# Kernel tuning notes

Measured on AMD Instinct MI355X. Metric: run time of the kernel, lower is better.

Reference implementation:

```python
import jax, jax.numpy as jnp
import numpy as np

B, T = 16384, 128  # batch, n_frames


def setup_inputs() -> dict:
    key = jax.random.key(0)
    k0, k1, k2, k3, k4, k5 = jax.random.split(key, 6)
    dir = jax.random.normal(k0, (B, 3), dtype=jnp.float32)
    R = jax.random.normal(k1, (B, T, 3, 3), dtype=jnp.float32)
    s = 1.0 / np.sqrt(3.0)  # torch LSTM default init scale (uniform +-1/sqrt(hidden))
    W_ih = jax.random.uniform(k2, (12, 3), jnp.float32, -s, s)
    W_hh = jax.random.uniform(k3, (12, 3), jnp.float32, -s, s)
    b_ih = jax.random.uniform(k4, (12,), jnp.float32, -s, s)
    b_hh = jax.random.uniform(k5, (12,), jnp.float32, -s, s)
    return {"dir": dir, "R": R, "W_ih": W_ih, "W_hh": W_hh, "b_ih": b_ih, "b_hh": b_hh}


def _rot_step(v, Rm):
    # v: [B,3], Rm: [B,3,3] -> Rm @ v
    nv = jnp.einsum('bij,bj->bi', Rm, v)
    return nv, nv


def _build_dirs(dir, R):
    n_frames = R.shape[1]
    half = n_frames // 2
    # Backward chain: dirs[i] = R[half-1-i]^T @ ... @ R[half-1]^T @ dir
    Rt_back = jnp.swapaxes(jnp.flip(R[:, :half], axis=1), 2, 3)  # [B, half, 3, 3]
    _, back = jax.lax.scan(_rot_step, dir, jnp.swapaxes(Rt_back, 0, 1))  # [half, B, 3]
    # Forward chain: dirs[i] = R[i-1] @ ... @ R[half] @ dir for i in half+1..n-1
    Rf = jnp.swapaxes(R[:, half:n_frames - 1], 0, 1)  # [n-1-half, B, 3, 3]
    _, fwd = jax.lax.scan(_rot_step, dir, Rf)  # [n-1-half, B, 3]
    dirs_tm = jnp.concatenate([back, dir[None], fwd], axis=0)  # time-major [T, B, 3]
    return dirs_tm, half


def _lstm(dirs_tm, W_ih, W_hh, b_ih, b_hh):
    Bsz = dirs_tm.shape[1]
    h0 = jnp.zeros((Bsz, 3), dirs_tm.dtype)
    c0 = jnp.zeros((Bsz, 3), dirs_tm.dtype)
    bias = b_ih + b_hh

    def step(carry, x):
        h, c = carry
        gates = x @ W_ih.T + h @ W_hh.T + bias  # [B,12]
        i = jax.nn.sigmoid(gates[:, 0:3])
        f = jax.nn.sigmoid(gates[:, 3:6])
        g = jnp.tanh(gates[:, 6:9])
        o = jax.nn.sigmoid(gates[:, 9:12])
        c = f * c + i * g
        h = o * jnp.tanh(c)
        return (h, c), h

    _, h_seq = jax.lax.scan(step, (h0, c0), dirs_tm)  # [T, B, 3]
    return h_seq


def reference(dir, R, W_ih, W_hh, b_ih, b_hh):
    dirs_tm, half = _build_dirs(dir, R)
    h_seq = _lstm(dirs_tm, W_ih, W_hh, b_ih, b_hh)
    dirs_out = jnp.swapaxes(dirs_tm, 0, 1)  # [B, T, 3]
    return dirs_out.at[:, half, :].set(h_seq[half])
```

## Files before the change

kernel.cpp:

```cpp
#include <hip/hip_runtime.h>

typedef float f4 __attribute__((ext_vector_type(4)));
typedef float f4u __attribute__((ext_vector_type(4), aligned(4)));

struct M3 { float m[3][3]; };

#define ELEM(q, n) ((q)[(n) >> 2][(n) & 3])

__device__ __forceinline__ M3 matmul(const M3& A, const M3& B) {
  M3 C;
#pragma unroll
  for (int i = 0; i < 3; ++i)
#pragma unroll
    for (int j = 0; j < 3; ++j)
      C.m[i][j] = A.m[i][0]*B.m[0][j] + A.m[i][1]*B.m[1][j] + A.m[i][2]*B.m[2][j];
  return C;
}

__device__ __forceinline__ M3 mk18(const f4 (&q)[18], int k) {
  M3 A;
#pragma unroll
  for (int i = 0; i < 3; ++i)
#pragma unroll
    for (int j = 0; j < 3; ++j)
      A.m[i][j] = ELEM(q, 9*k + 3*i + j);
  return A;
}

template <int CTRL>
__device__ __forceinline__ float dppf(float v) {
  return __int_as_float(
      __builtin_amdgcn_mov_dpp(__float_as_int(v), CTRL, 0xf, 0xf, true));
}

template <int D>
__device__ __forceinline__ M3 dpp_shr_mat(const M3& A) {
  M3 C;
#pragma unroll
  for (int i = 0; i < 3; ++i)
#pragma unroll
    for (int j = 0; j < 3; ++j)
      C.m[i][j] = dppf<0x110 + D>(A.m[i][j]);
  return C;
}

__device__ __forceinline__ float sigm(float z) {
  return __builtin_amdgcn_rcpf(1.0f + __expf(-z));
}
__device__ __forceinline__ float tanh_(float z) {
  float e = __expf(2.0f * z);
  return 1.0f - 2.0f * __builtin_amdgcn_rcpf(e + 1.0f);
}

template <int CTRL>
__device__ __forceinline__ float quad_bcast(float v) {
  return __int_as_float(
      __builtin_amdgcn_mov_dpp(__float_as_int(v), CTRL, 0xf, 0xf, true));
}

__global__ __launch_bounds__(128, 2) void fused_kernel(
    const float* __restrict__ dir, const float* __restrict__ R,
    const float* __restrict__ Wih, const float* __restrict__ Whh,
    const float* __restrict__ bih, const float* __restrict__ bhh,
    float* __restrict__ out, int B) {
  __shared__ __align__(16) f4 xrows[64 * 16];

  const int tid = threadIdx.x;
  const int lane = tid & 63;
  const int e = tid >> 3;
  const int s = tid & 7;
  const int b0 = blockIdx.x * 16;
  const int b = b0 + e;
  const bool valid = (b < B);
  const int bc = valid ? b : (B - 1);
  const f4* Rb4 = (const f4*)(R + (size_t)bc * 1152);

  f4 q[18], qf[18];
  {
    const f4* pb = Rb4 + 18 * (7 - s);
    const f4* pf = Rb4 + 144 + 18 * s;
#pragma unroll
    for (int i = 0; i < 18; ++i) q[i] = pb[i];
#pragma unroll
    for (int i = 0; i < 18; ++i) qf[i] = pf[i];
  }
#pragma unroll
  for (int i = 0; i < 18; ++i) asm volatile("" :: "v"(q[i]));
#pragma unroll
  for (int i = 0; i < 18; ++i) asm volatile("" :: "v"(qf[i]));

  const float d0 = dir[3*bc+0], d1 = dir[3*bc+1], d2 = dir[3*bc+2];

  {
    M3 P = mk18(q, 0);
#pragma unroll
    for (int k = 1; k < 8; ++k) P = matmul(mk18(q, k), P);

    M3 I = P;
    {
      M3 Sh = dpp_shr_mat<1>(I); M3 T = matmul(Sh, I);
#pragma unroll
      for (int i = 0; i < 3; ++i)
#pragma unroll
        for (int j = 0; j < 3; ++j) I.m[i][j] = (s >= 1) ? T.m[i][j] : I.m[i][j];
    }
    {
      M3 Sh = dpp_shr_mat<2>(I); M3 T = matmul(Sh, I);
#pragma unroll
      for (int i = 0; i < 3; ++i)
#pragma unroll
        for (int j = 0; j < 3; ++j) I.m[i][j] = (s >= 2) ? T.m[i][j] : I.m[i][j];
    }
    {
      M3 Sh = dpp_shr_mat<4>(I); M3 T = matmul(Sh, I);
#pragma unroll
      for (int i = 0; i < 3; ++i)
#pragma unroll
        for (int j = 0; j < 3; ++j) I.m[i][j] = (s >= 4) ? T.m[i][j] : I.m[i][j];
    }

    float w0 = I.m[0][0]*d0 + I.m[1][0]*d1 + I.m[2][0]*d2;
    float w1 = I.m[0][1]*d0 + I.m[1][1]*d1 + I.m[2][1]*d2;
    float w2 = I.m[0][2]*d0 + I.m[1][2]*d1 + I.m[2][2]*d2;
    float p0 = dppf<0x111>(w0), p1 = dppf<0x111>(w1), p2 = dppf<0x111>(w2);
    float v0 = (s == 0) ? d0 : p0;
    float v1 = (s == 0) ? d1 : p1;
    float v2 = (s == 0) ? d2 : p2;

    float row[24];
#pragma unroll
    for (int j = 0; j < 8; ++j) {
      M3 A = mk18(q, 7 - j);
      float n0 = v0*A.m[0][0] + v1*A.m[1][0] + v2*A.m[2][0];
      float n1 = v0*A.m[0][1] + v1*A.m[1][1] + v2*A.m[2][1];
      float n2 = v0*A.m[0][2] + v1*A.m[1][2] + v2*A.m[2][2];
      v0 = n0; v1 = n1; v2 = n2;
      row[3*j+0] = n0; row[3*j+1] = n1; row[3*j+2] = n2;
    }

    if (valid) {
      float* ob = out + (size_t)b * 384 + 24 * s;
#pragma unroll
      for (int kk = 0; kk < 6; ++kk) {
        f4 vv = { row[4*kk+0], row[4*kk+1], row[4*kk+2], row[4*kk+3] };
        ((f4*)ob)[kk] = vv;
      }
    }
#pragma unroll
    for (int j = 0; j < 8; ++j) {
      f4 vv = { row[3*j+0], row[3*j+1], row[3*j+2], 0.f };
      xrows[(8*s + j) * 16 + e] = vv;
    }
  }

  {
    M3 P = mk18(qf, 0);
#pragma unroll
    for (int k = 1; k < 8; ++k) P = matmul(mk18(qf, k), P);

    M3 I = P;
    {
      M3 Sh = dpp_shr_mat<1>(I); M3 T = matmul(I, Sh);
#pragma unroll
      for (int i = 0; i < 3; ++i)
#pragma unroll
        for (int j = 0; j < 3; ++j) I.m[i][j] = (s >= 1) ? T.m[i][j] : I.m[i][j];
    }
    {
      M3 Sh = dpp_shr_mat<2>(I); M3 T = matmul(I, Sh);
#pragma unroll
      for (int i = 0; i < 3; ++i)
#pragma unroll
        for (int j = 0; j < 3; ++j) I.m[i][j] = (s >= 2) ? T.m[i][j] : I.m[i][j];
    }
    {
      M3 Sh = dpp_shr_mat<4>(I); M3 T = matmul(I, Sh);
#pragma unroll
      for (int i = 0; i < 3; ++i)
#pragma unroll
        for (int j = 0; j < 3; ++j) I.m[i][j] = (s >= 4) ? T.m[i][j] : I.m[i][j];
    }

    float w0 = I.m[0][0]*d0 + I.m[0][1]*d1 + I.m[0][2]*d2;
    float w1 = I.m[1][0]*d0 + I.m[1][1]*d1 + I.m[1][2]*d2;
    float w2 = I.m[2][0]*d0 + I.m[2][1]*d1 + I.m[2][2]*d2;
    float p0 = dppf<0x111>(w0), p1 = dppf<0x111>(w1), p2 = dppf<0x111>(w2);
    float v0 = (s == 0) ? d0 : p0;
    float v1 = (s == 0) ? d1 : p1;
    float v2 = (s == 0) ? d2 : p2;

    float row[24];
#pragma unroll
    for (int j = 0; j < 8; ++j) {
      M3 A = mk18(qf, j);
      float n0 = A.m[0][0]*v0 + A.m[0][1]*v1 + A.m[0][2]*v2;
      float n1 = A.m[1][0]*v0 + A.m[1][1]*v1 + A.m[1][2]*v2;
      float n2 = A.m[2][0]*v0 + A.m[2][1]*v1 + A.m[2][2]*v2;
      v0 = n0; v1 = n1; v2 = n2;
      row[3*j+0] = n0; row[3*j+1] = n1; row[3*j+2] = n2;
    }

    if (valid) {
      float* ob = out + (size_t)b * 384 + (size_t)(65 + 8*s) * 3;
#pragma unroll
      for (int kk = 0; kk < 5; ++kk) {
        f4u vv = { row[4*kk+0], row[4*kk+1], row[4*kk+2], row[4*kk+3] };
        *(f4u*)(ob + 4*kk) = vv;
      }
      ob[20] = row[20];
      if (s < 7) { ob[21] = row[21]; ob[22] = row[22]; ob[23] = row[23]; }
    }
  }

  __syncthreads();
  if (tid >= 64) return;

  const int e2 = lane >> 2;
  const int u = lane & 3, uu = (u == 3) ? 0 : u;
  const int b2 = b0 + e2;
  const bool valid2 = (b2 < B);
  const int b2c = valid2 ? b2 : 0;

  const float wii0 = Wih[uu*3+0],     wii1 = Wih[uu*3+1],     wii2 = Wih[uu*3+2];
  const float wif0 = Wih[(3+uu)*3+0], wif1 = Wih[(3+uu)*3+1], wif2 = Wih[(3+uu)*3+2];
  const float wig0 = Wih[(6+uu)*3+0], wig1 = Wih[(6+uu)*3+1], wig2 = Wih[(6+uu)*3+2];
  const float wio0 = Wih[(9+uu)*3+0], wio1 = Wih[(9+uu)*3+1], wio2 = Wih[(9+uu)*3+2];
  const float whi0 = Whh[uu*3+0],     whi1 = Whh[uu*3+1],     whi2 = Whh[uu*3+2];
  const float whf0 = Whh[(3+uu)*3+0], whf1 = Whh[(3+uu)*3+1], whf2 = Whh[(3+uu)*3+2];
  const float whg0 = Whh[(6+uu)*3+0], whg1 = Whh[(6+uu)*3+1], whg2 = Whh[(6+uu)*3+2];
  const float who0 = Whh[(9+uu)*3+0], who1 = Whh[(9+uu)*3+1], who2 = Whh[(9+uu)*3+2];
  const float bsi = bih[uu]   + bhh[uu];
  const float bsf = bih[3+uu] + bhh[3+uu];
  const float bsg = bih[6+uu] + bhh[6+uu];
  const float bso = bih[9+uu] + bhh[9+uu];
  const float dd0 = dir[3*b2c+0], dd1 = dir[3*b2c+1], dd2 = dir[3*b2c+2];

  float h0 = 0.f, h1 = 0.f, h2 = 0.f, cc = 0.f, hl = 0.f;

#define LSTEP(x0_, x1_, x2_)                                                  \
  {                                                                           \
    float zi = bsi + wii0*(x0_) + wii1*(x1_) + wii2*(x2_)                     \
                   + whi0*h0 + whi1*h1 + whi2*h2;                             \
    float zf = bsf + wif0*(x0_) + wif1*(x1_) + wif2*(x2_)                     \
                   + whf0*h0 + whf1*h1 + whf2*h2;                             \
    float zg = bsg + wig0*(x0_) + wig1*(x1_) + wig2*(x2_)                     \
                   + whg0*h0 + whg1*h1 + whg2*h2;                             \
    float zo = bso + wio0*(x0_) + wio1*(x1_) + wio2*(x2_)                     \
                   + who0*h0 + who1*h1 + who2*h2;                             \
    float ai = sigm(zi), af = sigm(zf), ag = tanh_(zg), ao = sigm(zo);        \
    cc = af*cc + ai*ag;                                                       \
    float hn = ao * tanh_(cc);                                                \
    hl = hn;                                                                  \
    h0 = quad_bcast<0x00>(hn);                                                \
    h1 = quad_bcast<0x55>(hn);                                                \
    h2 = quad_bcast<0xAA>(hn);                                                \
  }

#pragma unroll 1
  for (int c = 0; c < 8; ++c) {
    f4 xa[8];
#pragma unroll
    for (int j = 0; j < 8; ++j) xa[j] = xrows[(c * 8 + j) * 16 + e2];
#pragma unroll
    for (int j = 0; j < 8; ++j) LSTEP(xa[j][0], xa[j][1], xa[j][2]);
  }
  LSTEP(dd0, dd1, dd2);
#undef LSTEP

  if (valid2 && u < 3) out[(size_t)b2 * 384 + 192 + u] = hl;
}

extern "C" void kernel_launch(void* const* d_in, const int* in_sizes, int n_in,
                              void* d_out, int out_size, void* d_ws, size_t ws_size,
                              hipStream_t stream) {
  const float* dir = (const float*)d_in[0];
  const float* R   = (const float*)d_in[1];
  const float* Wih = (const float*)d_in[2];
  const float* Whh = (const float*)d_in[3];
  const float* bih = (const float*)d_in[4];
  const float* bhh = (const float*)d_in[5];
  float* out = (float*)d_out;

  const int B = in_sizes[0] / 3;
  const int grid = (B + 15) / 16;
  hipLaunchKernelGGL(fused_kernel, dim3(grid), dim3(128), 0, stream,
                     dir, R, Wih, Whh, bih, bhh, out, B);
}
```

Baseline: 42.65 us.

## Use single-wave blocks with a four-iteration loop and register prefetch of R

```diff
diff --git a/kernel.cpp b/kernel.cpp
--- a/kernel.cpp
+++ b/kernel.cpp
@@ -58,162 +58,144 @@
       __builtin_amdgcn_mov_dpp(__float_as_int(v), CTRL, 0xf, 0xf, true));
 }
 
-__global__ __launch_bounds__(128, 2) void fused_kernel(
+__global__ __launch_bounds__(64) void fused_kernel(
     const float* __restrict__ dir, const float* __restrict__ R,
     const float* __restrict__ Wih, const float* __restrict__ Whh,
     const float* __restrict__ bih, const float* __restrict__ bhh,
     float* __restrict__ out, int B) {
   __shared__ __align__(16) f4 xrows[64 * 16];
 
-  const int tid = threadIdx.x;
-  const int lane = tid & 63;
-  const int e = tid >> 3;
-  const int s = tid & 7;
+  const int lane = threadIdx.x;
+  const int e8 = lane >> 3;
+  const int s = lane & 7;
   const int b0 = blockIdx.x * 16;
-  const int b = b0 + e;
-  const bool valid = (b < B);
-  const int bc = valid ? b : (B - 1);
-  const f4* Rb4 = (const f4*)(R + (size_t)bc * 1152);
-
-  f4 q[18], qf[18];
+
+  f4 qN[18];
   {
-    const f4* pb = Rb4 + 18 * (7 - s);
-    const f4* pf = Rb4 + 144 + 18 * s;
-#pragma unroll
-    for (int i = 0; i < 18; ++i) q[i] = pb[i];
-#pragma unroll
-    for (int i = 0; i < 18; ++i) qf[i] = pf[i];
-  }
-#pragma unroll
-  for (int i = 0; i < 18; ++i) asm volatile("" :: "v"(q[i]));
-#pragma unroll
-  for (int i = 0; i < 18; ++i) asm volatile("" :: "v"(qf[i]));
-
-  const float d0 = dir[3*bc+0], d1 = dir[3*bc+1], d2 = dir[3*bc+2];
-
-  {
+    int bn = b0 + e8; bn = (bn < B) ? bn : (B - 1);
+    const f4* p = (const f4*)(R + (size_t)bn * 1152) + 18 * (7 - s);
+#pragma unroll
+    for (int i = 0; i < 18; ++i) qN[i] = p[i];
+  }
+
+#pragma unroll 1
+  for (int it = 0; it < 4; ++it) {
+    const int g = it >> 1;
+    const int phase = it & 1;
+    const int b = b0 + g * 8 + e8;
+    const bool valid = (b < B);
+    const int bc = valid ? b : (B - 1);
+
+    f4 q[18];
+#pragma unroll
+    for (int i = 0; i < 18; ++i) q[i] = qN[i];
+
+    if (it < 3) {
+      const int itn = it + 1;
+      int bn = b0 + (itn >> 1) * 8 + e8; bn = (bn < B) ? bn : (B - 1);
+      const f4* p = (const f4*)(R + (size_t)bn * 1152) +
+                    ((itn & 1) ? (144 + 18 * s) : (18 * (7 - s)));
+#pragma unroll
+      for (int i = 0; i < 18; ++i) qN[i] = p[i];
+    }
+
+    const float d0 = dir[3*bc+0], d1 = dir[3*bc+1], d2 = dir[3*bc+2];
+
     M3 P = mk18(q, 0);
 #pragma unroll
     for (int k = 1; k < 8; ++k) P = matmul(mk18(q, k), P);
 
     M3 I = P;
     {
-      M3 Sh = dpp_shr_mat<1>(I); M3 T = matmul(Sh, I);
+      M3 Sh = dpp_shr_mat<1>(I);
+      M3 T; if (phase == 0) T = matmul(Sh, I); else T = matmul(I, Sh);
 #pragma unroll
       for (int i = 0; i < 3; ++i)
 #pragma unroll
         for (int j = 0; j < 3; ++j) I.m[i][j] = (s >= 1) ? T.m[i][j] : I.m[i][j];
     }
     {
-      M3 Sh = dpp_shr_mat<2>(I); M3 T = matmul(Sh, I);
+      M3 Sh = dpp_shr_mat<2>(I);
+      M3 T; if (phase == 0) T = matmul(Sh, I); else T = matmul(I, Sh);
 #pragma unroll
       for (int i = 0; i < 3; ++i)
 #pragma unroll
         for (int j = 0; j < 3; ++j) I.m[i][j] = (s >= 2) ? T.m[i][j] : I.m[i][j];
     }
     {
-      M3 Sh = dpp_shr_mat<4>(I); M3 T = matmul(Sh, I);
+      M3 Sh = dpp_shr_mat<4>(I);
+      M3 T; if (phase == 0) T = matmul(Sh, I); else T = matmul(I, Sh);
 #pragma unroll
       for (int i = 0; i < 3; ++i)
 #pragma unroll
         for (int j = 0; j < 3; ++j) I.m[i][j] = (s >= 4) ? T.m[i][j] : I.m[i][j];
     }
 
-    float w0 = I.m[0][0]*d0 + I.m[1][0]*d1 + I.m[2][0]*d2;
-    float w1 = I.m[0][1]*d0 + I.m[1][1]*d1 + I.m[2][1]*d2;
-    float w2 = I.m[0][2]*d0 + I.m[1][2]*d1 + I.m[2][2]*d2;
-    float p0 = dppf<0x111>(w0), p1 = dppf<0x111>(w1), p2 = dppf<0x111>(w2);
-    float v0 = (s == 0) ? d0 : p0;
-    float v1 = (s == 0) ? d1 : p1;
-    float v2 = (s == 0) ? d2 : p2;
-
-    float row[24];
-#pragma unroll
-    for (int j = 0; j < 8; ++j) {
-      M3 A = mk18(q, 7 - j);
-      float n0 = v0*A.m[0][0] + v1*A.m[1][0] + v2*A.m[2][0];
-      float n1 = v0*A.m[0][1] + v1*A.m[1][1] + v2*A.m[2][1];
-      float n2 = v0*A.m[0][2] + v1*A.m[1][2] + v2*A.m[2][2];
-      v0 = n0; v1 = n1; v2 = n2;
-      row[3*j+0] = n0; row[3*j+1] = n1; row[3*j+2] = n2;
-    }
-
-    if (valid) {
-      float* ob = out + (size_t)b * 384 + 24 * s;
-#pragma unroll
-      for (int kk = 0; kk < 6; ++kk) {
-        f4 vv = { row[4*kk+0], row[4*kk+1], row[4*kk+2], row[4*kk+3] };
-        ((f4*)ob)[kk] = vv;
-      }
-    }
-#pragma unroll
-    for (int j = 0; j < 8; ++j) {
-      f4 vv = { row[3*j+0], row[3*j+1], row[3*j+2], 0.f };
-      xrows[(8*s + j) * 16 + e] = vv;
-    }
-  }
-
-  {
-    M3 P = mk18(qf, 0);
-#pragma unroll
-    for (int k = 1; k < 8; ++k) P = matmul(mk18(qf, k), P);
-
-    M3 I = P;
-    {
-      M3 Sh = dpp_shr_mat<1>(I); M3 T = matmul(I, Sh);
-#pragma unroll
-      for (int i = 0; i < 3; ++i)
-#pragma unroll
-        for (int j = 0; j < 3; ++j) I.m[i][j] = (s >= 1) ? T.m[i][j] : I.m[i][j];
-    }
-    {
-      M3 Sh = dpp_shr_mat<2>(I); M3 T = matmul(I, Sh);
-#pragma unroll
-      for (int i = 0; i < 3; ++i)
-#pragma unroll
-        for (int j = 0; j < 3; ++j) I.m[i][j] = (s >= 2) ? T.m[i][j] : I.m[i][j];
-    }
-    {
-      M3 Sh = dpp_shr_mat<4>(I); M3 T = matmul(I, Sh);
-#pragma unroll
-      for (int i = 0; i < 3; ++i)
-#pragma unroll
-        for (int j = 0; j < 3; ++j) I.m[i][j] = (s >= 4) ? T.m[i][j] : I.m[i][j];
-    }
-
-    float w0 = I.m[0][0]*d0 + I.m[0][1]*d1 + I.m[0][2]*d2;
-    float w1 = I.m[1][0]*d0 + I.m[1][1]*d1 + I.m[1][2]*d2;
-    float w2 = I.m[2][0]*d0 + I.m[2][1]*d1 + I.m[2][2]*d2;
-    float p0 = dppf<0x111>(w0), p1 = dppf<0x111>(w1), p2 = dppf<0x111>(w2);
-    float v0 = (s == 0) ? d0 : p0;
-    float v1 = (s == 0) ? d1 : p1;
-    float v2 = (s == 0) ? d2 : p2;
-
-    float row[24];
-#pragma unroll
-    for (int j = 0; j < 8; ++j) {
-      M3 A = mk18(qf, j);
-      float n0 = A.m[0][0]*v0 + A.m[0][1]*v1 + A.m[0][2]*v2;
-      float n1 = A.m[1][0]*v0 + A.m[1][1]*v1 + A.m[1][2]*v2;
-      float n2 = A.m[2][0]*v0 + A.m[2][1]*v1 + A.m[2][2]*v2;
-      v0 = n0; v1 = n1; v2 = n2;
-      row[3*j+0] = n0; row[3*j+1] = n1; row[3*j+2] = n2;
-    }
-
-    if (valid) {
-      float* ob = out + (size_t)b * 384 + (size_t)(65 + 8*s) * 3;
-#pragma unroll
-      for (int kk = 0; kk < 5; ++kk) {
-        f4u vv = { row[4*kk+0], row[4*kk+1], row[4*kk+2], row[4*kk+3] };
-        *(f4u*)(ob + 4*kk) = vv;
-      }
-      ob[20] = row[20];
-      if (s < 7) { ob[21] = row[21]; ob[22] = row[22]; ob[23] = row[23]; }
-    }
-  }
-
-  __syncthreads();
-  if (tid >= 64) return;
+    if (phase == 0) {
+      float w0 = I.m[0][0]*d0 + I.m[1][0]*d1 + I.m[2][0]*d2;
+      float w1 = I.m[0][1]*d0 + I.m[1][1]*d1 + I.m[2][1]*d2;
+      float w2 = I.m[0][2]*d0 + I.m[1][2]*d1 + I.m[2][2]*d2;
+      float p0 = dppf<0x111>(w0), p1 = dppf<0x111>(w1), p2 = dppf<0x111>(w2);
+      float v0 = (s == 0) ? d0 : p0;
+      float v1 = (s == 0) ? d1 : p1;
+      float v2 = (s == 0) ? d2 : p2;
+
+      float row[24];
+#pragma unroll
+      for (int j = 0; j < 8; ++j) {
+        M3 A = mk18(q, 7 - j);
+        float n0 = v0*A.m[0][0] + v1*A.m[1][0] + v2*A.m[2][0];
+        float n1 = v0*A.m[0][1] + v1*A.m[1][1] + v2*A.m[2][1];
+        float n2 = v0*A.m[0][2] + v1*A.m[1][2] + v2*A.m[2][2];
+        v0 = n0; v1 = n1; v2 = n2;
+        row[3*j+0] = n0; row[3*j+1] = n1; row[3*j+2] = n2;
+      }
+
+      if (valid) {
+        float* ob = out + (size_t)b * 384 + 24 * s;
+#pragma unroll
+        for (int kk = 0; kk < 6; ++kk) {
+          f4 vv = { row[4*kk+0], row[4*kk+1], row[4*kk+2], row[4*kk+3] };
+          ((f4*)ob)[kk] = vv;
+        }
+      }
+#pragma unroll
+      for (int j = 0; j < 8; ++j) {
+        f4 vv = { row[3*j+0], row[3*j+1], row[3*j+2], 0.f };
+        xrows[(8*s + j) * 16 + g * 8 + e8] = vv;
+      }
+    } else {
+      float w0 = I.m[0][0]*d0 + I.m[0][1]*d1 + I.m[0][2]*d2;
+      float w1 = I.m[1][0]*d0 + I.m[1][1]*d1 + I.m[1][2]*d2;
+      float w2 = I.m[2][0]*d0 + I.m[2][1]*d1 + I.m[2][2]*d2;
+      float p0 = dppf<0x111>(w0), p1 = dppf<0x111>(w1), p2 = dppf<0x111>(w2);
+      float v0 = (s == 0) ? d0 : p0;
+      float v1 = (s == 0) ? d1 : p1;
+      float v2 = (s == 0) ? d2 : p2;
+
+      float row[24];
+#pragma unroll
+      for (int j = 0; j < 8; ++j) {
+        M3 A = mk18(q, j);
+        float n0 = A.m[0][0]*v0 + A.m[0][1]*v1 + A.m[0][2]*v2;
+        float n1 = A.m[1][0]*v0 + A.m[1][1]*v1 + A.m[1][2]*v2;
+        float n2 = A.m[2][0]*v0 + A.m[2][1]*v1 + A.m[2][2]*v2;
+        v0 = n0; v1 = n1; v2 = n2;
+        row[3*j+0] = n0; row[3*j+1] = n1; row[3*j+2] = n2;
+      }
+
+      if (valid) {
+        float* ob = out + (size_t)b * 384 + (size_t)(65 + 8*s) * 3;
+#pragma unroll
+        for (int kk = 0; kk < 5; ++kk) {
+          f4u vv = { row[4*kk+0], row[4*kk+1], row[4*kk+2], row[4*kk+3] };
+          *(f4u*)(ob + 4*kk) = vv;
+        }
+        ob[20] = row[20];
+        if (s < 7) { ob[21] = row[21]; ob[22] = row[22]; ob[23] = row[23]; }
+      }
+    }
+  }
 
   const int e2 = lane >> 2;
   const int u = lane & 3, uu = (u == 3) ? 0 : u;
@@ -283,6 +265,6 @@
 
   const int B = in_sizes[0] / 3;
   const int grid = (B + 15) / 16;
-  hipLaunchKernelGGL(fused_kernel, dim3(grid), dim3(128), 0, stream,
+  hipLaunchKernelGGL(fused_kernel, dim3(grid), dim3(64), 0, stream,
                      dir, R, Wih, Whh, bih, bhh, out, B);
 }
```

Measured after the change: 34.38 us. -19.4%, faster.
